# Performance work log

Hardware: AMD Instinct MI355X
Metric: run time of the kernel (lower is better)

## Reference

```python
import jax, jax.numpy as jnp
import numpy as np

N = 500_000   # points
V = 65_536    # voxels
C_IN = 6
GF = 64
OUT = 256


def setup_inputs() -> dict:
    key = jax.random.key(0)
    ks = jax.random.split(key, 14)
    p = lambda k, shape: (jax.random.normal(k, shape, jnp.float32) * 0.05)
    return {
        "inp_feat": jax.random.normal(ks[0], (N, C_IN), jnp.float32),
        "vox2point_idx": jax.random.randint(ks[1], (N,), 0, V, jnp.int64),
        "W1": p(ks[2], (C_IN, GF)),        "b1": p(ks[3], (GF,)),
        "W2": p(ks[4], (GF, OUT // 2)),    "b2": p(ks[5], (OUT // 2,)),
        "Wv1": p(ks[6], (OUT // 2, OUT // 2)), "bv1": p(ks[7], (OUT // 2,)),
        "W3": p(ks[8], (OUT, OUT)),        "b3": p(ks[9], (OUT,)),
        "W4": p(ks[10], (OUT, OUT)),       "b4": p(ks[11], (OUT,)),
        "Wv2": p(ks[12], (OUT, OUT)),      "bv2": p(ks[13], (OUT,)),
    }


def _segment_max0(x, idx, num_segments):
    # torch_scatter scatter(..., reduce='max') initializes empty slots to 0
    s = jax.ops.segment_max(x, idx, num_segments=num_segments)
    return jnp.where(jnp.isfinite(s), s, jnp.zeros((), x.dtype))


def reference(inp_feat, vox2point_idx, W1, b1, W2, b2, Wv1, bv1, W3, b3, W4, b4, Wv2, bv2):
    relu = jax.nn.relu
    point_feat1 = relu(inp_feat @ W1 + b1)            # [N, 64]
    point_feat2 = relu(point_feat1 @ W2 + b2)         # [N, 128]
    occ_voxel_feat = _segment_max0(point_feat2, vox2point_idx, V)   # [V, 128]
    occ_voxel_feat = relu(occ_voxel_feat @ Wv1 + bv1)               # [V, 128]
    point_global_feat = occ_voxel_feat[vox2point_idx]               # [N, 128] gather
    point_feat3 = jnp.concatenate([point_global_feat, point_feat2], axis=-1)  # [N, 256]
    point_feat4 = relu(point_feat3 @ W3 + b3)         # [N, 256]
    point_feat5 = relu(point_feat4 @ W4 + b4)         # [N, 256]
    occ_voxel_feat2 = _segment_max0(point_feat5, vox2point_idx, V)  # [V, 256]
    occ_voxel_feat2 = relu(occ_voxel_feat2 @ Wv2 + bv2)             # [V, 256]
    return occ_voxel_feat2
```

## Files before the change

### kernel.cpp

```cpp
#include <hip/hip_runtime.h>
#include <hip/hip_bf16.h>
#include <stdint.h>

#define N_PTS 500000
#define NVOX  65536
#define K1_TILES ((N_PTS + 127) / 128)
#define K3_TILES ((N_PTS + 63) / 64)

typedef __attribute__((ext_vector_type(8))) short bf16x8;
typedef __attribute__((ext_vector_type(4))) float f32x4;

__device__ inline unsigned short f2bf(float f) {
    union { float f; unsigned int u; } v; v.f = f;
    unsigned int r = v.u + 0x7FFFu + ((v.u >> 16) & 1u);
    return (unsigned short)(r >> 16);
}
__device__ inline float bf2f(unsigned short h) {
    return __uint_as_float((unsigned int)h << 16);
}

#define WOFF_W1T   0
#define WOFF_W2T   2048
#define WOFF_WV1T  10240
#define WOFF_W3AT  26624
#define WOFF_W3BT  59392
#define WOFF_W4T   92160
#define WOFF_WV2T  157696
#define W_TOTAL    223232

__global__ void prep_all(const float* __restrict__ W1, const float* __restrict__ W2,
                         const float* __restrict__ Wv1, const float* __restrict__ W3,
                         const float* __restrict__ W4, const float* __restrict__ Wv2,
                         unsigned short* __restrict__ dst) {
    int i = blockIdx.x * 256 + threadIdx.x;
    if (i >= W_TOTAL) return;
    int o = i;
    if (o < 2048) {
        int n = o >> 5, k = o & 31;
        dst[i] = (k < 6) ? f2bf(W1[k * 64 + n]) : (unsigned short)0;
    } else if ((o -= 2048) < 8192) {
        int n = o >> 6, k = o & 63;
        dst[i] = f2bf(W2[k * 128 + n]);
    } else if ((o -= 8192) < 16384) {
        int n = o >> 7, k = o & 127;
        dst[i] = f2bf(Wv1[k * 128 + n]);
    } else if ((o -= 16384) < 32768) {
        int n = o >> 7, k = o & 127;
        dst[i] = f2bf(W3[k * 256 + n]);
    } else if ((o -= 32768) < 32768) {
        int n = o >> 7, k = o & 127;
        dst[i] = f2bf(W3[(k + 128) * 256 + n]);
    } else if ((o -= 32768) < 65536) {
        int n = o >> 8, k = o & 255;
        dst[i] = f2bf(W4[k * 256 + n]);
    } else {
        o -= 65536;
        int n = o >> 8, k = o & 255;
        dst[i] = f2bf(Wv2[k * 256 + n]);
    }
}

__global__ void s_hist(const int* __restrict__ idx, unsigned int* __restrict__ counts) {
    int p = blockIdx.x * 256 + threadIdx.x;
    if (p < N_PTS) atomicAdd(&counts[idx[p]], 1u);
}

__global__ __launch_bounds__(1024) void s_scan(const unsigned int* __restrict__ counts,
                                               unsigned int* __restrict__ cursor) {
    __shared__ unsigned int sPart[1024];
    int t = threadIdx.x;
    unsigned int sum = 0;
    #pragma unroll 8
    for (int i = 0; i < 64; i++) sum += counts[t * 64 + i];
    sPart[t] = sum;
    __syncthreads();
    for (int d = 1; d < 1024; d <<= 1) {
        unsigned int add = (t >= d) ? sPart[t - d] : 0u;
        __syncthreads();
        sPart[t] += add;
        __syncthreads();
    }
    unsigned int run = (t == 0) ? 0u : sPart[t - 1];
    #pragma unroll 8
    for (int i = 0; i < 64; i++) {
        cursor[t * 64 + i] = run;
        run += counts[t * 64 + i];
    }
}

__global__ void s_scatter(const int* __restrict__ idx, unsigned int* __restrict__ cursor,
                          int* __restrict__ order, int* __restrict__ svox) {
    int p = blockIdx.x * 256 + threadIdx.x;
    if (p < N_PTS) {
        int v = idx[p];
        unsigned int pos = atomicAdd(&cursor[v], 1u);
        order[pos] = p;
        svox[pos] = v;
    }
}

__global__ __launch_bounds__(256) void k1_points(
    const float* __restrict__ inp,
    const int* __restrict__ order, const int* __restrict__ svox,
    const unsigned short* __restrict__ W1T, const float* __restrict__ b1,
    const unsigned short* __restrict__ W2T, const float* __restrict__ b2,
    unsigned int* __restrict__ vox1acc,
    unsigned short* __restrict__ feat2seq)
{
    __shared__ __align__(16) char sBuf[32 * 1024];
    __shared__ float sb1[64];
    __shared__ float sb2[128];
    __shared__ int   sVox[128];
    char* sIn = sBuf;
    char* sF1 = sBuf + 8 * 1024;
    char* sF2 = sBuf;
    const f32x4 fzero = {0.f, 0.f, 0.f, 0.f};
    int tid = threadIdx.x;
    int pbase = blockIdx.x * 128;
    if (tid < 64)       sb1[tid] = b1[tid];
    else if (tid < 192) sb2[tid - 64] = b2[tid - 64];
    if (tid < 128) {
        int i = pbase + tid;
        int pt = -1, v = -1;
        if (i < N_PTS) { pt = order[i]; v = svox[i]; }
        sVox[tid] = v;
        uint4 g0 = {0u, 0u, 0u, 0u};
        if (pt >= 0) {
            const float* x = inp + (size_t)pt * 6;
            g0.x = (unsigned)f2bf(x[0]) | ((unsigned)f2bf(x[1]) << 16);
            g0.y = (unsigned)f2bf(x[2]) | ((unsigned)f2bf(x[3]) << 16);
            g0.z = (unsigned)f2bf(x[4]) | ((unsigned)f2bf(x[5]) << 16);
        }
        int swz = (tid & 3) << 4;
        char* row = sIn + tid * 64;
        uint4 z = {0u, 0u, 0u, 0u};
        *(uint4*)(row + (0  ^ swz)) = g0;
        *(uint4*)(row + (16 ^ swz)) = z;
        *(uint4*)(row + (32 ^ swz)) = z;
        *(uint4*)(row + (48 ^ swz)) = z;
    }
    __syncthreads();
    int wave = tid >> 6, lane = tid & 63, quad = lane >> 4, l16 = lane & 15;

    {
        f32x4 acc1[8];
        #pragma unroll
        for (int mt = 0; mt < 8; mt++) acc1[mt] = fzero;
        int n = wave * 16 + l16;
        bf16x8 b = *(const bf16x8*)(W1T + n * 32 + quad * 8);
        #pragma unroll
        for (int mt = 0; mt < 8; mt++) {
            int m = mt * 16 + l16;
            bf16x8 a = *(const bf16x8*)(sIn + m * 64 + ((quad * 16) ^ ((m & 3) << 4)));
            acc1[mt] = __builtin_amdgcn_mfma_f32_16x16x32_bf16(a, b, acc1[mt], 0, 0, 0);
        }
        float bias = sb1[n];
        #pragma unroll
        for (int mt = 0; mt < 8; mt++)
            #pragma unroll
            for (int r = 0; r < 4; r++) {
                int m = mt * 16 + quad * 4 + r;
                float v = fmaxf(acc1[mt][r] + bias, 0.f);
                *(unsigned short*)(sF1 + m * 128 + ((2 * n) ^ ((m & 7) << 4))) = f2bf(v);
            }
    }
    __syncthreads();
    f32x4 acc2[2][8];
    #pragma unroll
    for (int j = 0; j < 2; j++)
        #pragma unroll
        for (int mt = 0; mt < 8; mt++) acc2[j][mt] = fzero;
    #pragma unroll
    for (int kt = 0; kt < 2; kt++) {
        bf16x8 b0 = *(const bf16x8*)(W2T + ((wave * 2 + 0) * 16 + l16) * 64 + kt * 32 + quad * 8);
        bf16x8 b1 = *(const bf16x8*)(W2T + ((wave * 2 + 1) * 16 + l16) * 64 + kt * 32 + quad * 8);
        #pragma unroll
        for (int mt = 0; mt < 8; mt++) {
            int m = mt * 16 + l16;
            bf16x8 a = *(const bf16x8*)(sF1 + m * 128 + ((kt * 64 + quad * 16) ^ ((m & 7) << 4)));
            acc2[0][mt] = __builtin_amdgcn_mfma_f32_16x16x32_bf16(a, b0, acc2[0][mt], 0, 0, 0);
            acc2[1][mt] = __builtin_amdgcn_mfma_f32_16x16x32_bf16(a, b1, acc2[1][mt], 0, 0, 0);
        }
    }
    __syncthreads();
    #pragma unroll
    for (int j = 0; j < 2; j++) {
        int n = (wave * 2 + j) * 16 + l16;
        float bias = sb2[n];
        #pragma unroll
        for (int mt = 0; mt < 8; mt++)
            #pragma unroll
            for (int r = 0; r < 4; r++) {
                int m = mt * 16 + quad * 4 + r;
                float v = fmaxf(acc2[j][mt][r] + bias, 0.f);
                *(unsigned short*)(sF2 + m * 256 + ((2 * n) ^ ((m & 7) << 4))) = f2bf(v);
            }
    }
    __syncthreads();
    if (feat2seq) {
        #pragma unroll
        for (int it = 0; it < 8; it++) {
            int i = tid + 256 * it;
            int m = i >> 4, q = i & 15;
            if (pbase + m < N_PTS) {
                uint4 val = *(const uint4*)(sF2 + m * 256 + ((q * 16) ^ ((m & 7) << 4)));
                *(uint4*)(feat2seq + (size_t)(pbase + m) * 128 + q * 8) = val;
            }
        }
    }
    {
        int c = tid & 127, r0 = (tid >> 7) * 64;
        int cur = -1; float vmax = 0.f; int segStart = r0;
        for (int r = r0; r < r0 + 64; r++) {
            int v = sVox[r];
            float f = bf2f(*(const unsigned short*)(sF2 + r * 256 + ((2 * c) ^ ((r & 7) << 4))));
            if (v != cur) {
                if (cur >= 0) {
                    if (segStart > r0)
                        vox1acc[(size_t)cur * 128 + c] = __float_as_uint(vmax);
                    else
                        atomicMax(vox1acc + (size_t)cur * 128 + c, __float_as_uint(vmax));
                }
                cur = v; vmax = f; segStart = r;
            } else vmax = fmaxf(vmax, f);
        }
        if (cur >= 0)
            atomicMax(vox1acc + (size_t)cur * 128 + c, __float_as_uint(vmax));
    }
}

__global__ __launch_bounds__(256) void kvox2(
    const float* __restrict__ in, const unsigned short* __restrict__ Wv1T,
    const float* __restrict__ bv1, const unsigned short* __restrict__ W3aT,
    unsigned short* __restrict__ voxB)
{
    __shared__ __align__(16) char sA[64 * 256];
    __shared__ __align__(16) char sB[64 * 256];
    __shared__ float sb[128];
    const f32x4 fzero = {0.f, 0.f, 0.f, 0.f};
    int tid = threadIdx.x;
    int vb = blockIdx.x * 64;
    if (tid < 128) sb[tid] = bv1[tid];
    #pragma unroll
    for (int it = 0; it < 8; it++) {
        int i = tid + 256 * it;
        int m = i >> 5, kq = i & 31;
        float4 f = ((const float4*)(in + (size_t)(vb + m) * 128))[kq];
        uint2 p;
        p.x = (unsigned)f2bf(f.x) | ((unsigned)f2bf(f.y) << 16);
        p.y = (unsigned)f2bf(f.z) | ((unsigned)f2bf(f.w) << 16);
        *(uint2*)(sA + m * 256 + ((8 * kq) ^ ((m & 7) << 4))) = p;
    }
    __syncthreads();
    int wave = tid >> 6, lane = tid & 63, quad = lane >> 4, l16 = lane & 15;
    {
        f32x4 acc[2][4];
        #pragma unroll
        for (int j = 0; j < 2; j++)
            #pragma unroll
            for (int mt = 0; mt < 4; mt++) acc[j][mt] = fzero;
        #pragma unroll
        for (int kt = 0; kt < 4; kt++) {
            bf16x8 a[4];
            #pragma unroll
            for (int mt = 0; mt < 4; mt++) {
                int m = mt * 16 + l16;
                a[mt] = *(const bf16x8*)(sA + m * 256 + ((kt * 64 + quad * 16) ^ ((m & 7) << 4)));
            }
            #pragma unroll
            for (int j = 0; j < 2; j++) {
                int n = (wave * 2 + j) * 16 + l16;
                bf16x8 b = *(const bf16x8*)(Wv1T + n * 128 + kt * 32 + quad * 8);
                #pragma unroll
                for (int mt = 0; mt < 4; mt++)
                    acc[j][mt] = __builtin_amdgcn_mfma_f32_16x16x32_bf16(a[mt], b, acc[j][mt], 0, 0, 0);
            }
        }
        #pragma unroll
        for (int j = 0; j < 2; j++) {
            int n = (wave * 2 + j) * 16 + l16;
            float bi = sb[n];
            #pragma unroll
            for (int mt = 0; mt < 4; mt++)
                #pragma unroll
                for (int r = 0; r < 4; r++) {
                    int m = mt * 16 + quad * 4 + r;
                    float v = fmaxf(acc[j][mt][r] + bi, 0.f);
                    *(unsigned short*)(sB + m * 256 + ((2 * n) ^ ((m & 7) << 4))) = f2bf(v);
                }
        }
    }
    __syncthreads();
    {
        f32x4 acc[4][4];
        #pragma unroll
        for (int j = 0; j < 4; j++)
            #pragma unroll
            for (int mt = 0; mt < 4; mt++) acc[j][mt] = fzero;
        #pragma unroll
        for (int kt = 0; kt < 4; kt++) {
            bf16x8 a[4];
            #pragma unroll
            for (int mt = 0; mt < 4; mt++) {
                int m = mt * 16 + l16;
                a[mt] = *(const bf16x8*)(sB + m * 256 + ((kt * 64 + quad * 16) ^ ((m & 7) << 4)));
            }
            #pragma unroll
            for (int j = 0; j < 4; j++) {
                int n = (wave * 4 + j) * 16 + l16;
                bf16x8 b = *(const bf16x8*)(W3aT + n * 128 + kt * 32 + quad * 8);
                #pragma unroll
                for (int mt = 0; mt < 4; mt++)
                    acc[j][mt] = __builtin_amdgcn_mfma_f32_16x16x32_bf16(a[mt], b, acc[j][mt], 0, 0, 0);
            }
        }
        #pragma unroll
        for (int j = 0; j < 4; j++) {
            int n = (wave * 4 + j) * 16 + l16;
            #pragma unroll
            for (int mt = 0; mt < 4; mt++)
                #pragma unroll
                for (int r = 0; r < 4; r++) {
                    int m = mt * 16 + quad * 4 + r;
                    voxB[(size_t)(vb + m) * 256 + n] = f2bf(acc[j][mt][r]);
                }
        }
    }
}

__global__ __launch_bounds__(256, 3) void k3_lite(
    const int* __restrict__ svox,
    const unsigned short* __restrict__ feat2seq,
    const unsigned short* __restrict__ voxB,
    const unsigned short* __restrict__ W3bT, const float* __restrict__ b3,
    const unsigned short* __restrict__ W4T, const float* __restrict__ b4,
    unsigned int* __restrict__ vox2acc)
{
    __shared__ __align__(16) char sBuf[48 * 1024];
    __shared__ float sb3[256];
    __shared__ float sb4[256];
    __shared__ int   sVox[64];
    char* sP  = sBuf;
    char* sF2 = sBuf + 32 * 1024;
    const f32x4 fzero = {0.f, 0.f, 0.f, 0.f};
    int tid = threadIdx.x;
    int pbase = blockIdx.x * 64;
    sb3[tid] = b3[tid];
    sb4[tid] = b4[tid];
    if (tid < 64) {
        int i = pbase + tid;
        sVox[tid] = (i < N_PTS) ? svox[i] : -1;
    }
    #pragma unroll
    for (int it = 0; it < 4; it++) {
        int i = tid + 256 * it;
        int m = i >> 4, q = i & 15;
        uint4 val = {0u, 0u, 0u, 0u};
        if (pbase + m < N_PTS)
            val = ((const uint4*)(feat2seq + (size_t)(pbase + m) * 128))[q];
        *(uint4*)(sF2 + m * 256 + ((q * 16) ^ ((m & 7) << 4))) = val;
    }
    #pragma unroll
    for (int it = 0; it < 8; it++) {
        int i = tid + 256 * it;
        int m = i >> 5, c = i & 31;
        uint4 val = {0u, 0u, 0u, 0u};
        int p = pbase + m;
        if (p < N_PTS) {
            int vv = svox[p];
            val = ((const uint4*)(voxB + (size_t)vv * 256))[c];
        }
        *(uint4*)(sP + m * 512 + ((c * 16) ^ ((m & 7) << 4))) = val;
    }
    __syncthreads();
    int wave = tid >> 6, lane = tid & 63, quad = lane >> 4, l16 = lane & 15;

    f32x4 acc[4][4];
    #pragma unroll
    for (int j = 0; j < 4; j++)
        #pragma unroll
        for (int mt = 0; mt < 4; mt++) acc[j][mt] = fzero;
    #pragma unroll 1
    for (int kt = 0; kt < 4; kt++) {
        bf16x8 a[4];
        #pragma unroll
        for (int mt = 0; mt < 4; mt++) {
            int m = mt * 16 + l16;
            a[mt] = *(const bf16x8*)(sF2 + m * 256 + ((kt * 64 + quad * 16) ^ ((m & 7) << 4)));
        }
        #pragma unroll
        for (int j = 0; j < 4; j++) {
            int n = (wave * 4 + j) * 16 + l16;
            bf16x8 b = *(const bf16x8*)(W3bT + n * 128 + kt * 32 + quad * 8);
            #pragma unroll
            for (int mt = 0; mt < 4; mt++)
                acc[j][mt] = __builtin_amdgcn_mfma_f32_16x16x32_bf16(a[mt], b, acc[j][mt], 0, 0, 0);
        }
    }
    #pragma unroll
    for (int j = 0; j < 4; j++) {
        int n = (wave * 4 + j) * 16 + l16;
        float bias = sb3[n];
        #pragma unroll
        for (int mt = 0; mt < 4; mt++)
            #pragma unroll
            for (int r = 0; r < 4; r++) {
                int m = mt * 16 + quad * 4 + r;
                char* p = sP + m * 512 + ((2 * n) ^ ((m & 7) << 4));
                float vox = bf2f(*(const unsigned short*)p);
                float v = fmaxf(acc[j][mt][r] + bias + vox, 0.f);
                *(unsigned short*)p = f2bf(v);
            }
    }
    __syncthreads();
    #pragma unroll
    for (int j = 0; j < 4; j++)
        #pragma unroll
        for (int mt = 0; mt < 4; mt++) acc[j][mt] = fzero;
    #pragma unroll 1
    for (int kt = 0; kt < 8; kt++) {
        bf16x8 a[4];
        #pragma unroll
        for (int mt = 0; mt < 4; mt++) {
            int m = mt * 16 + l16;
            a[mt] = *(const bf16x8*)(sP + m * 512 + ((kt * 64 + quad * 16) ^ ((m & 7) << 4)));
        }
        #pragma unroll
        for (int j = 0; j < 4; j++) {
            int n = (wave * 4 + j) * 16 + l16;
            bf16x8 b = *(const bf16x8*)(W4T + n * 256 + kt * 32 + quad * 8);
            #pragma unroll
            for (int mt = 0; mt < 4; mt++)
                acc[j][mt] = __builtin_amdgcn_mfma_f32_16x16x32_bf16(a[mt], b, acc[j][mt], 0, 0, 0);
        }
    }
    __syncthreads();
    #pragma unroll
    for (int j = 0; j < 4; j++) {
        int n = (wave * 4 + j) * 16 + l16;
        float bias = sb4[n];
        #pragma unroll
        for (int mt = 0; mt < 4; mt++)
            #pragma unroll
            for (int r = 0; r < 4; r++) {
                int m = mt * 16 + quad * 4 + r;
                float v = fmaxf(acc[j][mt][r] + bias, 0.f);
                *(unsigned short*)(sP + m * 512 + ((2 * n) ^ ((m & 7) << 4))) = f2bf(v);
            }
    }
    __syncthreads();
    {
        int c = tid;
        int cur = -1; float vmax = 0.f; int segStart = 0;
        for (int r = 0; r < 64; r++) {
            int v = sVox[r];
            float f = bf2f(*(const unsigned short*)(sP + r * 512 + ((2 * c) ^ ((r & 7) << 4))));
            if (v != cur) {
                if (cur >= 0) {
                    if (segStart > 0)
                        vox2acc[(size_t)cur * 256 + c] = __float_as_uint(vmax);
                    else
                        atomicMax(vox2acc + (size_t)cur * 256 + c, __float_as_uint(vmax));
                }
                cur = v; vmax = f; segStart = r;
            } else vmax = fmaxf(vmax, f);
        }
        if (cur >= 0)
            atomicMax(vox2acc + (size_t)cur * 256 + c, __float_as_uint(vmax));
    }
}

__global__ __launch_bounds__(256, 3) void k3_heavy(
    const float* __restrict__ inp,
    const int* __restrict__ order, const int* __restrict__ svox,
    const unsigned short* __restrict__ W1T, const float* __restrict__ b1,
    const unsigned short* __restrict__ W2T, const float* __restrict__ b2,
    const unsigned short* __restrict__ voxB,
    const unsigned short* __restrict__ W3bT, const float* __restrict__ b3,
    const unsigned short* __restrict__ W4T, const float* __restrict__ b4,
    unsigned int* __restrict__ vox2acc)
{
    __shared__ __align__(16) char sBuf[32 * 1024];
    __shared__ float sb1[64];
    __shared__ float sb2[128];
    __shared__ float sb3[256];
    __shared__ float sb4[256];
    __shared__ int   sVox[64];
    char* sF2 = sBuf;
    char* sF1 = sBuf + 16 * 1024;
    char* sIn = sBuf + 24 * 1024;
    char* sP  = sBuf;
    const f32x4 fzero = {0.f, 0.f, 0.f, 0.f};
    int tid = threadIdx.x;
    int pbase = blockIdx.x * 64;
    sb3[tid] = b3[tid];
    sb4[tid] = b4[tid];
    if (tid < 64)  sb1[tid] = b1[tid];
    if (tid < 128) sb2[tid] = b2[tid];
    if (tid < 64) {
        int i = pbase + tid;
        int pt = -1, v = -1;
        if (i < N_PTS) { pt = order[i]; v = svox[i]; }
        sVox[tid] = v;
        uint4 g0 = {0u, 0u, 0u, 0u};
        if (pt >= 0) {
            const float* x = inp + (size_t)pt * 6;
            g0.x = (unsigned)f2bf(x[0]) | ((unsigned)f2bf(x[1]) << 16);
            g0.y = (unsigned)f2bf(x[2]) | ((unsigned)f2bf(x[3]) << 16);
            g0.z = (unsigned)f2bf(x[4]) | ((unsigned)f2bf(x[5]) << 16);
        }
        int swz = (tid & 3) << 4;
        char* row = sIn + tid * 64;
        uint4 z = {0u, 0u, 0u, 0u};
        *(uint4*)(row + (0  ^ swz)) = g0;
        *(uint4*)(row + (16 ^ swz)) = z;
        *(uint4*)(row + (32 ^ swz)) = z;
        *(uint4*)(row + (48 ^ swz)) = z;
    }
    __syncthreads();
    int wave = tid >> 6, lane = tid & 63, quad = lane >> 4, l16 = lane & 15;

    {
        f32x4 acc1[4];
        #pragma unroll
        for (int mt = 0; mt < 4; mt++) acc1[mt] = fzero;
        int n = wave * 16 + l16;
        bf16x8 b = *(const bf16x8*)(W1T + n * 32 + quad * 8);
        #pragma unroll
        for (int mt = 0; mt < 4; mt++) {
            int m = mt * 16 + l16;
            bf16x8 a = *(const bf16x8*)(sIn + m * 64 + ((quad * 16) ^ ((m & 3) << 4)));
            acc1[mt] = __builtin_amdgcn_mfma_f32_16x16x32_bf16(a, b, acc1[mt], 0, 0, 0);
        }
        float bias = sb1[n];
        #pragma unroll
        for (int mt = 0; mt < 4; mt++)
            #pragma unroll
            for (int r = 0; r < 4; r++) {
                int m = mt * 16 + quad * 4 + r;
                float v = fmaxf(acc1[mt][r] + bias, 0.f);
                *(unsigned short*)(sF1 + m * 128 + ((2 * n) ^ ((m & 7) << 4))) = f2bf(v);
            }
    }
    __syncthreads();
    {
        f32x4 acc2[2][4];
        #pragma unroll
        for (int j = 0; j < 2; j++)
            #pragma unroll
            for (int mt = 0; mt < 4; mt++) acc2[j][mt] = fzero;
        #pragma unroll
        for (int kt = 0; kt < 2; kt++) {
            bf16x8 b0 = *(const bf16x8*)(W2T + ((wave * 2 + 0) * 16 + l16) * 64 + kt * 32 + quad * 8);
            bf16x8 b1 = *(const bf16x8*)(W2T + ((wave * 2 + 1) * 16 + l16) * 64 + kt * 32 + quad * 8);
            #pragma unroll
            for (int mt = 0; mt < 4; mt++) {
                int m = mt * 16 + l16;
                bf16x8 a = *(const bf16x8*)(sF1 + m * 128 + ((kt * 64 + quad * 16) ^ ((m & 7) << 4)));
                acc2[0][mt] = __builtin_amdgcn_mfma_f32_16x16x32_bf16(a, b0, acc2[0][mt], 0, 0, 0);
                acc2[1][mt] = __builtin_amdgcn_mfma_f32_16x16x32_bf16(a, b1, acc2[1][mt], 0, 0, 0);
            }
        }
        #pragma unroll
        for (int j = 0; j < 2; j++) {
            int n = (wave * 2 + j) * 16 + l16;
            float bias = sb2[n];
            #pragma unroll
            for (int mt = 0; mt < 4; mt++)
                #pragma unroll
                for (int r = 0; r < 4; r++) {
                    int m = mt * 16 + quad * 4 + r;
                    float v = fmaxf(acc2[j][mt][r] + bias, 0.f);
                    *(unsigned short*)(sF2 + m * 256 + ((2 * n) ^ ((m & 7) << 4))) = f2bf(v);
                }
        }
    }
    __syncthreads();

    f32x4 acc[4][4];
    #pragma unroll
    for (int j = 0; j < 4; j++)
        #pragma unroll
        for (int mt = 0; mt < 4; mt++) acc[j][mt] = fzero;
    #pragma unroll 1
    for (int kt = 0; kt < 4; kt++) {
        bf16x8 a[4];
        #pragma unroll
        for (int mt = 0; mt < 4; mt++) {
            int m = mt * 16 + l16;
            a[mt] = *(const bf16x8*)(sF2 + m * 256 + ((kt * 64 + quad * 16) ^ ((m & 7) << 4)));
        }
        #pragma unroll
        for (int j = 0; j < 4; j++) {
            int n = (wave * 4 + j) * 16 + l16;
            bf16x8 b = *(const bf16x8*)(W3bT + n * 128 + kt * 32 + quad * 8);
            #pragma unroll
            for (int mt = 0; mt < 4; mt++)
                acc[j][mt] = __builtin_amdgcn_mfma_f32_16x16x32_bf16(a[mt], b, acc[j][mt], 0, 0, 0);
        }
    }
    __syncthreads();
    #pragma unroll
    for (int it = 0; it < 8; it++) {
        int i = tid + 256 * it;
        int m = i >> 5, c = i & 31;
        int vv = sVox[m];
        uint4 val = {0u, 0u, 0u, 0u};
        if (vv >= 0)
            val = ((const uint4*)(voxB + (size_t)vv * 256))[c];
        *(uint4*)(sP + m * 512 + ((c * 16) ^ ((m & 7) << 4))) = val;
    }
    __syncthreads();
    #pragma unroll
    for (int j = 0; j < 4; j++) {
        int n = (wave * 4 + j) * 16 + l16;
        float bias = sb3[n];
        #pragma unroll
        for (int mt = 0; mt < 4; mt++)
            #pragma unroll
            for (int r = 0; r < 4; r++) {
                int m = mt * 16 + quad * 4 + r;
                char* p = sP + m * 512 + ((2 * n) ^ ((m & 7) << 4));
                float vox = bf2f(*(const unsigned short*)p);
                float v = fmaxf(acc[j][mt][r] + bias + vox, 0.f);
                *(unsigned short*)p = f2bf(v);
            }
    }
    __syncthreads();
    #pragma unroll
    for (int j = 0; j < 4; j++)
        #pragma unroll
        for (int mt = 0; mt < 4; mt++) acc[j][mt] = fzero;
    #pragma unroll 1
    for (int kt = 0; kt < 8; kt++) {
        bf16x8 a[4];
        #pragma unroll
        for (int mt = 0; mt < 4; mt++) {
            int m = mt * 16 + l16;
            a[mt] = *(const bf16x8*)(sP + m * 512 + ((kt * 64 + quad * 16) ^ ((m & 7) << 4)));
        }
        #pragma unroll
        for (int j = 0; j < 4; j++) {
            int n = (wave * 4 + j) * 16 + l16;
            bf16x8 b = *(const bf16x8*)(W4T + n * 256 + kt * 32 + quad * 8);
            #pragma unroll
            for (int mt = 0; mt < 4; mt++)
                acc[j][mt] = __builtin_amdgcn_mfma_f32_16x16x32_bf16(a[mt], b, acc[j][mt], 0, 0, 0);
        }
    }
    __syncthreads();
    #pragma unroll
    for (int j = 0; j < 4; j++) {
        int n = (wave * 4 + j) * 16 + l16;
        float bias = sb4[n];
        #pragma unroll
        for (int mt = 0; mt < 4; mt++)
            #pragma unroll
            for (int r = 0; r < 4; r++) {
                int m = mt * 16 + quad * 4 + r;
                float v = fmaxf(acc[j][mt][r] + bias, 0.f);
                *(unsigned short*)(sP + m * 512 + ((2 * n) ^ ((m & 7) << 4))) = f2bf(v);
            }
    }
    __syncthreads();
    {
        int c = tid;
        int cur = -1; float vmax = 0.f; int segStart = 0;
        for (int r = 0; r < 64; r++) {
            int v = sVox[r];
            float f = bf2f(*(const unsigned short*)(sP + r * 512 + ((2 * c) ^ ((r & 7) << 4))));
            if (v != cur) {
                if (cur >= 0) {
                    if (segStart > 0)
                        vox2acc[(size_t)cur * 256 + c] = __float_as_uint(vmax);
                    else
                        atomicMax(vox2acc + (size_t)cur * 256 + c, __float_as_uint(vmax));
                }
                cur = v; vmax = f; segStart = r;
            } else vmax = fmaxf(vmax, f);
        }
        if (cur >= 0)
            atomicMax(vox2acc + (size_t)cur * 256 + c, __float_as_uint(vmax));
    }
}

__global__ __launch_bounds__(256) void kvox_final(
    const float* __restrict__ in, const unsigned short* __restrict__ WT,
    const float* __restrict__ bias, float* __restrict__ outp)
{
    __shared__ __align__(16) char sA[64 * 512];
    __shared__ float sb[256];
    const f32x4 fzero = {0.f, 0.f, 0.f, 0.f};
    int tid = threadIdx.x;
    int vb = blockIdx.x * 64;
    sb[tid] = bias[tid];
    #pragma unroll
    for (int it = 0; it < 16; it++) {
        int i = tid + 256 * it;
        int m = i >> 6, kq = i & 63;
        float4 f = ((const float4*)(in + (size_t)(vb + m) * 256))[kq];
        uint2 p;
        p.x = (unsigned)f2bf(f.x) | ((unsigned)f2bf(f.y) << 16);
        p.y = (unsigned)f2bf(f.z) | ((unsigned)f2bf(f.w) << 16);
        *(uint2*)(sA + m * 512 + ((8 * kq) ^ ((m & 7) << 4))) = p;
    }
    __syncthreads();
    int wave = tid >> 6, lane = tid & 63, quad = lane >> 4, l16 = lane & 15;
    f32x4 acc[4][4];
    #pragma unroll
    for (int j = 0; j < 4; j++)
        #pragma unroll
        for (int mt = 0; mt < 4; mt++) acc[j][mt] = fzero;
    #pragma unroll 1
    for (int kt = 0; kt < 8; kt++) {
        bf16x8 a[4];
        #pragma unroll
        for (int mt = 0; mt < 4; mt++) {
            int m = mt * 16 + l16;
            a[mt] = *(const bf16x8*)(sA + m * 512 + ((kt * 64 + quad * 16) ^ ((m & 7) << 4)));
        }
        #pragma unroll
        for (int j = 0; j < 4; j++) {
            int n = (wave * 4 + j) * 16 + l16;
            bf16x8 b = *(const bf16x8*)(WT + n * 256 + kt * 32 + quad * 8);
            #pragma unroll
            for (int mt = 0; mt < 4; mt++)
                acc[j][mt] = __builtin_amdgcn_mfma_f32_16x16x32_bf16(a[mt], b, acc[j][mt], 0, 0, 0);
        }
    }
    #pragma unroll
    for (int j = 0; j < 4; j++) {
        int n = (wave * 4 + j) * 16 + l16;
        float bi = sb[n];
        #pragma unroll
        for (int mt = 0; mt < 4; mt++)
            #pragma unroll
            for (int r = 0; r < 4; r++) {
                int m = mt * 16 + quad * 4 + r;
                outp[(size_t)(vb + m) * 256 + n] = fmaxf(acc[j][mt][r] + bi, 0.f);
            }
    }
}

extern "C" void kernel_launch(void* const* d_in, const int* in_sizes, int n_in,
                              void* d_out, int out_size, void* d_ws, size_t ws_size,
                              hipStream_t stream) {
    const float* inp  = (const float*)d_in[0];
    const int*   idx  = (const int*)d_in[1];
    const float* W1   = (const float*)d_in[2];
    const float* b1   = (const float*)d_in[3];
    const float* W2   = (const float*)d_in[4];
    const float* b2   = (const float*)d_in[5];
    const float* Wv1  = (const float*)d_in[6];
    const float* bv1  = (const float*)d_in[7];
    const float* W3   = (const float*)d_in[8];
    const float* b3   = (const float*)d_in[9];
    const float* W4   = (const float*)d_in[10];
    const float* b4   = (const float*)d_in[11];
    const float* Wv2  = (const float*)d_in[12];
    const float* bv2  = (const float*)d_in[13];

    char* ws = (char*)d_ws;
    size_t off = 0;
    unsigned int*   vox1acc = (unsigned int*)(ws + off);   off += (size_t)NVOX * 128 * 4;
    unsigned int*   counts  = (unsigned int*)(ws + off);   off += (size_t)NVOX * 4;
    unsigned int*   cursor  = (unsigned int*)(ws + off);   off += (size_t)NVOX * 4;
    int*            order   = (int*)(ws + off);            off += (size_t)N_PTS * 4;
    int*            svox    = (int*)(ws + off);            off += (size_t)N_PTS * 4;
    unsigned short* wsW     = (unsigned short*)(ws + off); off += (size_t)W_TOTAL * 2;

    unsigned short* feat2seq = nullptr;
    if (ws_size >= off + (size_t)N_PTS * 128 * 2)
        feat2seq = (unsigned short*)(ws + off);

    const unsigned short* W1T  = wsW + WOFF_W1T;
    const unsigned short* W2T  = wsW + WOFF_W2T;
    const unsigned short* Wv1T = wsW + WOFF_WV1T;
    const unsigned short* W3aT = wsW + WOFF_W3AT;
    const unsigned short* W3bT = wsW + WOFF_W3BT;
    const unsigned short* W4T  = wsW + WOFF_W4T;
    const unsigned short* Wv2T = wsW + WOFF_WV2T;

    unsigned short* voxB = (unsigned short*)vox1acc;
    unsigned int* vox2acc = (unsigned int*)d_out;

    hipMemsetAsync(vox1acc, 0, (size_t)NVOX * 128 * 4 + (size_t)NVOX * 4, stream);
    hipMemsetAsync(vox2acc, 0, (size_t)NVOX * 256 * 4, stream);

    prep_all<<<(W_TOTAL + 255) / 256, 256, 0, stream>>>(W1, W2, Wv1, W3, W4, Wv2, wsW);

    s_hist<<<(N_PTS + 255) / 256, 256, 0, stream>>>(idx, counts);
    s_scan<<<1, 1024, 0, stream>>>(counts, cursor);
    s_scatter<<<(N_PTS + 255) / 256, 256, 0, stream>>>(idx, cursor, order, svox);

    k1_points<<<K1_TILES, 256, 0, stream>>>(inp, order, svox, W1T, b1, W2T, b2,
                                            vox1acc, feat2seq);
    kvox2<<<NVOX / 64, 256, 0, stream>>>((const float*)vox1acc, Wv1T, bv1, W3aT, voxB);
    if (feat2seq)
        k3_lite<<<K3_TILES, 256, 0, stream>>>(svox, feat2seq, voxB,
                                              W3bT, b3, W4T, b4, vox2acc);
    else
        k3_heavy<<<K3_TILES, 256, 0, stream>>>(inp, order, svox, W1T, b1, W2T, b2, voxB,
                                               W3bT, b3, W4T, b4, vox2acc);
    kvox_final<<<NVOX / 64, 256, 0, stream>>>((const float*)vox2acc, Wv2T, bv2,
                                              (float*)d_out);
}
```

Before: 648.1 us.

## Shrink k3_lite LDS by staging half of gathered voxel rows in registers

```diff
diff --git a/kernel.cpp b/kernel.cpp
--- a/kernel.cpp
+++ b/kernel.cpp
@@ -99,7 +99,7 @@
     }
 }
 
-__global__ __launch_bounds__(256) void k1_points(
+__global__ __launch_bounds__(256, 4) void k1_points(
     const float* __restrict__ inp,
     const int* __restrict__ order, const int* __restrict__ svox,
     const unsigned short* __restrict__ W1T, const float* __restrict__ b1,
@@ -229,7 +229,7 @@
     }
 }
 
-__global__ __launch_bounds__(256) void kvox2(
+__global__ __launch_bounds__(256, 4) void kvox2(
     const float* __restrict__ in, const unsigned short* __restrict__ Wv1T,
     const float* __restrict__ bv1, const unsigned short* __restrict__ W3aT,
     unsigned short* __restrict__ voxB)
@@ -328,7 +328,7 @@
     }
 }
 
-__global__ __launch_bounds__(256, 3) void k3_lite(
+__global__ __launch_bounds__(256, 4) void k3_lite(
     const int* __restrict__ svox,
     const unsigned short* __restrict__ feat2seq,
     const unsigned short* __restrict__ voxB,
@@ -336,12 +336,12 @@
     const unsigned short* __restrict__ W4T, const float* __restrict__ b4,
     unsigned int* __restrict__ vox2acc)
 {
-    __shared__ __align__(16) char sBuf[48 * 1024];
+    __shared__ __align__(16) char sBuf[32 * 1024];
     __shared__ float sb3[256];
     __shared__ float sb4[256];
     __shared__ int   sVox[64];
     char* sP  = sBuf;
-    char* sF2 = sBuf + 32 * 1024;
+    char* sF2 = sBuf + 16 * 1024;
     const f32x4 fzero = {0.f, 0.f, 0.f, 0.f};
     int tid = threadIdx.x;
     int pbase = blockIdx.x * 64;
@@ -351,6 +351,33 @@
         int i = pbase + tid;
         sVox[tid] = (i < N_PTS) ? svox[i] : -1;
     }
+    uint4 h0 = {0u,0u,0u,0u}, h1 = {0u,0u,0u,0u}, h2 = {0u,0u,0u,0u}, h3 = {0u,0u,0u,0u};
+    {
+        int i = tid + 1024, m = i >> 5, c = i & 31, p = pbase + m;
+        if (p < N_PTS) h0 = ((const uint4*)(voxB + (size_t)svox[p] * 256))[c];
+    }
+    {
+        int i = tid + 1280, m = i >> 5, c = i & 31, p = pbase + m;
+        if (p < N_PTS) h1 = ((const uint4*)(voxB + (size_t)svox[p] * 256))[c];
+    }
+    {
+        int i = tid + 1536, m = i >> 5, c = i & 31, p = pbase + m;
+        if (p < N_PTS) h2 = ((const uint4*)(voxB + (size_t)svox[p] * 256))[c];
+    }
+    {
+        int i = tid + 1792, m = i >> 5, c = i & 31, p = pbase + m;
+        if (p < N_PTS) h3 = ((const uint4*)(voxB + (size_t)svox[p] * 256))[c];
+    }
+    #pragma unroll
+    for (int it = 0; it < 4; it++) {
+        int i = tid + 256 * it;
+        int m = i >> 5, c = i & 31;
+        uint4 val = {0u, 0u, 0u, 0u};
+        int p = pbase + m;
+        if (p < N_PTS)
+            val = ((const uint4*)(voxB + (size_t)svox[p] * 256))[c];
+        *(uint4*)(sP + m * 512 + ((c * 16) ^ ((m & 7) << 4))) = val;
+    }
     #pragma unroll
     for (int it = 0; it < 4; it++) {
         int i = tid + 256 * it;
@@ -360,18 +387,6 @@
             val = ((const uint4*)(feat2seq + (size_t)(pbase + m) * 128))[q];
         *(uint4*)(sF2 + m * 256 + ((q * 16) ^ ((m & 7) << 4))) = val;
     }
-    #pragma unroll
-    for (int it = 0; it < 8; it++) {
-        int i = tid + 256 * it;
-        int m = i >> 5, c = i & 31;
-        uint4 val = {0u, 0u, 0u, 0u};
-        int p = pbase + m;
-        if (p < N_PTS) {
-            int vv = svox[p];
-            val = ((const uint4*)(voxB + (size_t)vv * 256))[c];
-        }
-        *(uint4*)(sP + m * 512 + ((c * 16) ^ ((m & 7) << 4))) = val;
-    }
     __syncthreads();
     int wave = tid >> 6, lane = tid & 63, quad = lane >> 4, l16 = lane & 15;
 
@@ -397,6 +412,24 @@
                 acc[j][mt] = __builtin_amdgcn_mfma_f32_16x16x32_bf16(a[mt], b, acc[j][mt], 0, 0, 0);
         }
     }
+    __syncthreads();
+    {
+        int i = tid + 1024, m = i >> 5, c = i & 31;
+        *(uint4*)(sP + m * 512 + ((c * 16) ^ ((m & 7) << 4))) = h0;
+    }
+    {
+        int i = tid + 1280, m = i >> 5, c = i & 31;
+        *(uint4*)(sP + m * 512 + ((c * 16) ^ ((m & 7) << 4))) = h1;
+    }
+    {
+        int i = tid + 1536, m = i >> 5, c = i & 31;
+        *(uint4*)(sP + m * 512 + ((c * 16) ^ ((m & 7) << 4))) = h2;
+    }
+    {
+        int i = tid + 1792, m = i >> 5, c = i & 31;
+        *(uint4*)(sP + m * 512 + ((c * 16) ^ ((m & 7) << 4))) = h3;
+    }
+    __syncthreads();
     #pragma unroll
     for (int j = 0; j < 4; j++) {
         int n = (wave * 4 + j) * 16 + l16;
@@ -684,7 +717,7 @@
     }
 }
 
-__global__ __launch_bounds__(256) void kvox_final(
+__global__ __launch_bounds__(256, 4) void kvox_final(
     const float* __restrict__ in, const unsigned short* __restrict__ WT,
     const float* __restrict__ bias, float* __restrict__ outp)
 {
```

After: 680.9 us. 1.05x slower.

## Shrink k3_lite LDS via buffer aliasing and direct global-to-LDS loads

Applied to the files above, without the earlier changes.

```diff
diff --git a/kernel.cpp b/kernel.cpp
--- a/kernel.cpp
+++ b/kernel.cpp
@@ -17,6 +17,12 @@
 }
 __device__ inline float bf2f(unsigned short h) {
     return __uint_as_float((unsigned int)h << 16);
+}
+
+__device__ inline void gld16(const void* g, void* l) {
+    __builtin_amdgcn_global_load_lds(
+        (const __attribute__((address_space(1))) unsigned int*)g,
+        (__attribute__((address_space(3))) unsigned int*)l, 16, 0, 0);
 }
 
 #define WOFF_W1T   0
@@ -99,7 +105,7 @@
     }
 }
 
-__global__ __launch_bounds__(256) void k1_points(
+__global__ __launch_bounds__(256, 4) void k1_points(
     const float* __restrict__ inp,
     const int* __restrict__ order, const int* __restrict__ svox,
     const unsigned short* __restrict__ W1T, const float* __restrict__ b1,
@@ -229,7 +235,7 @@
     }
 }
 
-__global__ __launch_bounds__(256) void kvox2(
+__global__ __launch_bounds__(256, 4) void kvox2(
     const float* __restrict__ in, const unsigned short* __restrict__ Wv1T,
     const float* __restrict__ bv1, const unsigned short* __restrict__ W3aT,
     unsigned short* __restrict__ voxB)
@@ -328,7 +334,7 @@
     }
 }
 
-__global__ __launch_bounds__(256, 3) void k3_lite(
+__global__ __launch_bounds__(256, 4) void k3_lite(
     const int* __restrict__ svox,
     const unsigned short* __restrict__ feat2seq,
     const unsigned short* __restrict__ voxB,
@@ -336,15 +342,16 @@
     const unsigned short* __restrict__ W4T, const float* __restrict__ b4,
     unsigned int* __restrict__ vox2acc)
 {
-    __shared__ __align__(16) char sBuf[48 * 1024];
+    __shared__ __align__(16) char sBuf[32 * 1024];
     __shared__ float sb3[256];
     __shared__ float sb4[256];
     __shared__ int   sVox[64];
     char* sP  = sBuf;
-    char* sF2 = sBuf + 32 * 1024;
+    char* sF2 = sBuf + 16 * 1024;
     const f32x4 fzero = {0.f, 0.f, 0.f, 0.f};
     int tid = threadIdx.x;
     int pbase = blockIdx.x * 64;
+    int wave = tid >> 6, lane = tid & 63, quad = lane >> 4, l16 = lane & 15;
     sb3[tid] = b3[tid];
     sb4[tid] = b4[tid];
     if (tid < 64) {
@@ -352,28 +359,24 @@
         sVox[tid] = (i < N_PTS) ? svox[i] : -1;
     }
     #pragma unroll
-    for (int it = 0; it < 4; it++) {
-        int i = tid + 256 * it;
-        int m = i >> 4, q = i & 15;
-        uint4 val = {0u, 0u, 0u, 0u};
-        if (pbase + m < N_PTS)
-            val = ((const uint4*)(feat2seq + (size_t)(pbase + m) * 128))[q];
-        *(uint4*)(sF2 + m * 256 + ((q * 16) ^ ((m & 7) << 4))) = val;
-    }
-    #pragma unroll
-    for (int it = 0; it < 8; it++) {
-        int i = tid + 256 * it;
-        int m = i >> 5, c = i & 31;
-        uint4 val = {0u, 0u, 0u, 0u};
-        int p = pbase + m;
-        if (p < N_PTS) {
-            int vv = svox[p];
-            val = ((const uint4*)(voxB + (size_t)vv * 256))[c];
-        }
-        *(uint4*)(sP + m * 512 + ((c * 16) ^ ((m & 7) << 4))) = val;
-    }
-    __syncthreads();
-    int wave = tid >> 6, lane = tid & 63, quad = lane >> 4, l16 = lane & 15;
+    for (int i = 0; i < 4; i++) {
+        int q = wave * 4 + i;
+        int m = 2 * q + (lane >> 5);
+        int u = lane & 31;
+        int p = pbase + m; if (p >= N_PTS) p = N_PTS - 1;
+        gld16(voxB + (size_t)svox[p] * 256 + (size_t)(u ^ (m & 7)) * 8,
+              sP + q * 1024);
+    }
+    #pragma unroll
+    for (int i = 0; i < 4; i++) {
+        int q = wave * 4 + i;
+        int m = 4 * q + (lane >> 4);
+        int u = lane & 15;
+        int p = pbase + m; if (p >= N_PTS) p = N_PTS - 1;
+        gld16(feat2seq + (size_t)p * 128 + (size_t)(u ^ (m & 7)) * 8,
+              sF2 + q * 1024);
+    }
+    __syncthreads();
 
     f32x4 acc[4][4];
     #pragma unroll
@@ -397,6 +400,17 @@
                 acc[j][mt] = __builtin_amdgcn_mfma_f32_16x16x32_bf16(a[mt], b, acc[j][mt], 0, 0, 0);
         }
     }
+    __syncthreads();
+    #pragma unroll
+    for (int i = 0; i < 4; i++) {
+        int q = wave * 4 + i;
+        int m = 32 + 2 * q + (lane >> 5);
+        int u = lane & 31;
+        int p = pbase + m; if (p >= N_PTS) p = N_PTS - 1;
+        gld16(voxB + (size_t)svox[p] * 256 + (size_t)(u ^ (m & 7)) * 8,
+              sP + 16 * 1024 + q * 1024);
+    }
+    __syncthreads();
     #pragma unroll
     for (int j = 0; j < 4; j++) {
         int n = (wave * 4 + j) * 16 + l16;
@@ -684,7 +698,7 @@
     }
 }
 
-__global__ __launch_bounds__(256) void kvox_final(
+__global__ __launch_bounds__(256, 4) void kvox_final(
     const float* __restrict__ in, const unsigned short* __restrict__ WT,
     const float* __restrict__ bias, float* __restrict__ outp)
 {
```

New measurement: 663.9 us. 2.4% more time.
